# Kernel optimization log

Hardware: AMD Instinct MI355X
Metric: run time of the kernel (lower is better)

Reference implementation:

```python
import jax, jax.numpy as jnp
import numpy as np

N = 250_000        # nodes
E = 8_000_000      # directed edges
F_IN = 16          # dataset.num_features
H = 8              # latent_dim
G = 512            # number of graphs in the batch


def setup_inputs() -> dict:
    key = jax.random.key(0)
    k = jax.random.split(key, 9)
    x = jax.random.normal(k[0], (N, F_IN), dtype=jnp.float32)
    edge_index = jax.random.randint(k[1], (2, E), 0, N, dtype=jnp.int64)
    batch = jnp.sort(jax.random.randint(k[2], (N,), 0, G, dtype=jnp.int64))
    W1 = jax.random.normal(k[3], (F_IN, H), dtype=jnp.float32) * 0.25
    b1 = jax.random.normal(k[4], (H,), dtype=jnp.float32) * 0.1
    W2 = jax.random.normal(k[5], (H, H), dtype=jnp.float32) * 0.35
    b2 = jax.random.normal(k[6], (H,), dtype=jnp.float32) * 0.1
    Wl = jax.random.normal(k[7], (H, 1), dtype=jnp.float32) * 0.35
    bl = jax.random.normal(k[8], (1,), dtype=jnp.float32) * 0.1
    return {"x": x, "edge_index": edge_index, "batch": batch,
            "W1": W1, "b1": b1, "W2": W2, "b2": b2, "Wl": Wl, "bl": bl}


def _gcn_conv(x, src, dst, deg_inv_sqrt, W, b, num_nodes):
    # PyG GCNConv (default): h = x @ W ; msg = norm * h[src] ; scatter-add to dst ; + bias
    h = x @ W                                    # [N, H]
    norm = deg_inv_sqrt[src] * deg_inv_sqrt[dst]  # [E+N]
    msgs = h[src] * norm[:, None]                 # [E+N, H]
    out = jax.ops.segment_sum(msgs, dst, num_segments=num_nodes)
    return out + b


def reference(x, edge_index, batch, W1, b1, W2, b2, Wl, bl):
    num_nodes = x.shape[0]
    loops = jnp.arange(num_nodes, dtype=edge_index.dtype)
    src = jnp.concatenate([edge_index[0], loops])  # self-loops appended
    dst = jnp.concatenate([edge_index[1], loops])
    # symmetric normalization: deg over destination (incl. self-loops)
    deg = jax.ops.segment_sum(jnp.ones_like(dst, dtype=x.dtype), dst,
                              num_segments=num_nodes)
    dis = jnp.where(deg > 0, jax.lax.rsqrt(jnp.maximum(deg, 1.0)), 0.0)
    h = jax.nn.relu(_gcn_conv(x, src, dst, dis, W1, b1, num_nodes))
    h = jax.nn.relu(_gcn_conv(h, src, dst, dis, W2, b2, num_nodes))
    pooled = jax.ops.segment_sum(h, batch, num_segments=G)  # global_add_pool -> [G, H]
    return jax.nn.sigmoid(pooled @ Wl + bl)                 # [G, 1]
```

## Files before the change

kernel.cpp:

```cpp
#include <hip/hip_runtime.h>
#include <math.h>

#define BLK 256
#define CH 8192
#define NBMAX 1024


__global__ void k_init0(int* __restrict__ ghist, float* __restrict__ zacc,
                        int* __restrict__ rowptr, int nb, int ng, int n, int E,
                        int primary) {
  int i = blockIdx.x * BLK + threadIdx.x;
  if (i < nb) ghist[i] = 0;
  if (i < ng) zacc[i] = 0.f;
  if (primary && i == 0) rowptr[n] = E;
}

__global__ void k_hist(const int* __restrict__ dst, int* __restrict__ ghist,
                       int E, int nb, int chunk) {
  __shared__ int h[NBMAX];
  for (int i = threadIdx.x; i < NBMAX; i += BLK) h[i] = 0;
  __syncthreads();
  long long s0 = (long long)blockIdx.x * chunk;
  int c = (int)min((long long)chunk, (long long)E - s0);
  for (int i = threadIdx.x; i < c; i += BLK)
    atomicAdd(&h[dst[s0 + i] >> 8], 1);
  __syncthreads();
  for (int b = threadIdx.x; b < nb; b += BLK)
    if (h[b]) atomicAdd(&ghist[b], h[b]);
}

__global__ void k_scan(const int* __restrict__ ghist, int* __restrict__ base,
                       int* __restrict__ cursor, int nb, int E) {
  __shared__ int temp[BLK];
  int t = threadIdx.x;
  int v[4]; int sm = 0;
  #pragma unroll
  for (int k = 0; k < 4; ++k) {
    int idx = t * 4 + k;
    v[k] = (idx < nb) ? ghist[idx] : 0;
    sm += v[k];
  }
  temp[t] = sm; __syncthreads();
  int inc = sm;
  for (int off = 1; off < BLK; off <<= 1) {
    int u = (t >= off) ? temp[t - off] : 0; __syncthreads();
    inc += u; temp[t] = inc; __syncthreads();
  }
  int run = inc - sm;
  #pragma unroll
  for (int k = 0; k < 4; ++k) {
    int idx = t * 4 + k;
    if (idx < nb) { base[idx] = run; cursor[idx] = run; }
    run += v[k];
  }
  if (t == BLK - 1) base[nb] = E;
}

__global__ void k_bin(const int* __restrict__ src, const int* __restrict__ dst,
                      int* __restrict__ cursor, int* __restrict__ binned,
                      int E, int nb) {
  __shared__ int cnt[NBMAX], cur[NBMAX], gofs[NBMAX], baseA[NBMAX + 1], temp[BLK];
  __shared__ int stage[CH];
  int t = threadIdx.x;
  for (int i = t; i < NBMAX; i += BLK) { cnt[i] = 0; cur[i] = 0; }
  __syncthreads();
  long long s0 = (long long)blockIdx.x * CH;
  int c = (int)min((long long)CH, (long long)E - s0);
  for (int i = t; i < c; i += BLK) atomicAdd(&cnt[dst[s0 + i] >> 8], 1);
  __syncthreads();
  int v[4], sm = 0;
  #pragma unroll
  for (int k = 0; k < 4; ++k) { v[k] = cnt[t * 4 + k]; sm += v[k]; }
  temp[t] = sm; __syncthreads();
  int inc = sm;
  for (int off = 1; off < BLK; off <<= 1) {
    int u = (t >= off) ? temp[t - off] : 0; __syncthreads();
    inc += u; temp[t] = inc; __syncthreads();
  }
  int run = inc - sm;
  #pragma unroll
  for (int k = 0; k < 4; ++k) { baseA[t * 4 + k] = run; run += v[k]; }
  if (t == BLK - 1) baseA[NBMAX] = c;
  __syncthreads();
  for (int b = t; b < nb; b += BLK)
    if (cnt[b]) gofs[b] = atomicAdd(&cursor[b], cnt[b]);
  __syncthreads();
  for (int i = t; i < c; i += BLK) {
    int d = dst[s0 + i];
    int b = d >> 8;
    int r = atomicAdd(&cur[b], 1);
    stage[baseA[b] + r] = (src[s0 + i] << 8) | (d & 255);
  }
  __syncthreads();
  for (int i = t; i < c; i += BLK) {
    int lo = 0, hi = nb;
    while (hi - lo > 1) { int m = (lo + hi) >> 1; if (baseA[m] <= i) lo = m; else hi = m; }
    binned[(size_t)gofs[lo] + (i - baseA[lo])] = stage[i];
  }
}

__global__ void k_sortdis(const int* __restrict__ base, const int* __restrict__ binned,
                          int* __restrict__ csr, int* __restrict__ rowptr,
                          float* __restrict__ dis, int n) {
  __shared__ int cnt[256], loff[256], cur[256], temp[BLK];
  int b = blockIdx.x, t = threadIdx.x;
  cnt[t] = 0; cur[t] = 0;
  __syncthreads();
  int s = base[b], e = base[b + 1];
  for (int i = s + t; i < e; i += BLK) atomicAdd(&cnt[binned[i] & 255], 1);
  __syncthreads();
  int v = cnt[t];
  temp[t] = v; __syncthreads();
  int inc = v;
  for (int off = 1; off < BLK; off <<= 1) {
    int u = (t >= off) ? temp[t - off] : 0; __syncthreads();
    inc += u; temp[t] = inc; __syncthreads();
  }
  loff[t] = inc - v;
  int node = b * 256 + t;
  if (node < n) {
    rowptr[node] = s + inc - v;
    dis[node] = rsqrtf((float)(v + 1));
  }
  __syncthreads();
  for (int i = s + t; i < e; i += BLK) {
    int rec = binned[i];
    int L = rec & 255;
    int p = atomicAdd(&cur[L], 1);
    csr[s + loff[L] + p] = rec >> 8;
  }
}

__global__ void k_gather(const int* __restrict__ rowptr, const int* __restrict__ csr,
                         const float* __restrict__ y, float* __restrict__ acc, int n) {
  int t = blockIdx.x * BLK + threadIdx.x;
  int node = t >> 3;
  int h = t & 7;
  if (node >= n) return;
  int start = rowptr[node];
  int end = rowptr[node + 1];
  float s = 0.f;
  int si = (start < end) ? csr[start] : 0;
  for (int k = start; k < end; ++k) {
    int nsi = (k + 1 < end) ? csr[k + 1] : 0;
    s += y[(size_t)si * 8 + h];
    si = nsi;
  }
  acc[(size_t)node * 8 + h] = s;
}


__global__ void k_degdis(const int* __restrict__ base, const int* __restrict__ binned,
                         float* __restrict__ dis, int n) {
  __shared__ int deg[256];
  int b = blockIdx.x, t = threadIdx.x;
  deg[t] = 1;
  __syncthreads();
  int s = base[b], e = base[b + 1];
  for (int i = s + t; i < e; i += BLK) atomicAdd(&deg[binned[i] & 255], 1);
  __syncthreads();
  int node = b * 256 + t;
  if (node < n) dis[node] = rsqrtf((float)deg[t]);
}

__global__ void k_acc(const int* __restrict__ base, const int* __restrict__ binned,
                      const float* __restrict__ y, float* __restrict__ acc, int n) {
  __shared__ float fa[2048];
  int b = blockIdx.x, t = threadIdx.x;
  for (int i = t; i < 2048; i += BLK) fa[i] = 0.f;
  __syncthreads();
  int s = base[b], e = base[b + 1];
  int j = t & 7;
  for (int i = s + (t >> 3); i < e; i += 32) {
    int rec = binned[i];
    atomicAdd(&fa[(rec & 255) * 8 + j], y[(size_t)(rec >> 8) * 8 + j]);
  }
  __syncthreads();
  int node0 = b * 256;
  int lim = (n - node0 < 256 ? n - node0 : 256) * 8;
  for (int i = t; i < lim; i += BLK) acc[(size_t)node0 * 8 + i] = fa[i];
}


__global__ void k_y1n(const float* __restrict__ x, const float* __restrict__ W1,
                      const float* __restrict__ dis, float* __restrict__ y, int n) {
  __shared__ float sW[128];
  if (threadIdx.x < 128) sW[threadIdx.x] = W1[threadIdx.x];
  __syncthreads();
  int i = blockIdx.x * BLK + threadIdx.x;
  if (i >= n) return;
  const float4* xp = (const float4*)(x + (size_t)i * 16);
  float4 a = xp[0], bb = xp[1], cc = xp[2], d4 = xp[3];
  float xv[16] = {a.x,a.y,a.z,a.w, bb.x,bb.y,bb.z,bb.w,
                  cc.x,cc.y,cc.z,cc.w, d4.x,d4.y,d4.z,d4.w};
  float ds = dis[i];
  float o[8];
  #pragma unroll
  for (int jj = 0; jj < 8; ++jj) {
    float s = 0.f;
    #pragma unroll
    for (int k = 0; k < 16; ++k) s = fmaf(xv[k], sW[k*8 + jj], s);
    o[jj] = ds * s;
  }
  float4* yp = (float4*)(y + (size_t)i * 8);
  yp[0] = make_float4(o[0], o[1], o[2], o[3]);
  yp[1] = make_float4(o[4], o[5], o[6], o[7]);
}

__global__ void k_mid(const float* __restrict__ dis, float* __restrict__ y,
                      float* __restrict__ acc, const float* __restrict__ W2,
                      const float* __restrict__ b1, int n, int zero_acc) {
  __shared__ float sW[64];
  __shared__ float sb[8];
  if (threadIdx.x < 64) sW[threadIdx.x] = W2[threadIdx.x];
  if (threadIdx.x < 8)  sb[threadIdx.x] = b1[threadIdx.x];
  __syncthreads();
  int i = blockIdx.x * BLK + threadIdx.x;
  if (i >= n) return;
  float d = dis[i];
  float4* yp = (float4*)(y + (size_t)i * 8);
  float4* ap = (float4*)(acc + (size_t)i * 8);
  float4 y0 = yp[0], y1v = yp[1], a0 = ap[0], a1 = ap[1];
  float yy[8] = {y0.x,y0.y,y0.z,y0.w, y1v.x,y1v.y,y1v.z,y1v.w};
  float aa[8] = {a0.x,a0.y,a0.z,a0.w, a1.x,a1.y,a1.z,a1.w};
  float hv[8];
  #pragma unroll
  for (int jj = 0; jj < 8; ++jj) hv[jj] = fmaxf(fmaf(d, yy[jj] + aa[jj], sb[jj]), 0.f);
  float o[8];
  #pragma unroll
  for (int jj = 0; jj < 8; ++jj) {
    float s = 0.f;
    #pragma unroll
    for (int k = 0; k < 8; ++k) s = fmaf(hv[k], sW[k*8 + jj], s);
    o[jj] = d * s;
  }
  yp[0] = make_float4(o[0], o[1], o[2], o[3]);
  yp[1] = make_float4(o[4], o[5], o[6], o[7]);
  if (zero_acc) {
    ap[0] = make_float4(0.f, 0.f, 0.f, 0.f);
    ap[1] = make_float4(0.f, 0.f, 0.f, 0.f);
  }
}

__global__ void k_final(const float* __restrict__ dis, const float* __restrict__ y,
                        const float* __restrict__ acc, const float* __restrict__ b2,
                        const float* __restrict__ Wl, const int* __restrict__ batch,
                        float* __restrict__ zacc, int n) {
  __shared__ float sb[8], sw[8];
  if (threadIdx.x < 8) { sb[threadIdx.x] = b2[threadIdx.x]; sw[threadIdx.x] = Wl[threadIdx.x]; }
  __syncthreads();
  int i = blockIdx.x * BLK + threadIdx.x;
  float s = 0.f;
  int g = -1;
  if (i < n) {
    float d = dis[i];
    const float4* yp = (const float4*)(y + (size_t)i * 8);
    const float4* ap = (const float4*)(acc + (size_t)i * 8);
    float4 y0 = yp[0], y1v = yp[1], a0 = ap[0], a1 = ap[1];
    float yy[8] = {y0.x,y0.y,y0.z,y0.w, y1v.x,y1v.y,y1v.z,y1v.w};
    float aa[8] = {a0.x,a0.y,a0.z,a0.w, a1.x,a1.y,a1.z,a1.w};
    #pragma unroll
    for (int jj = 0; jj < 8; ++jj) {
      float h = fmaxf(fmaf(d, yy[jj] + aa[jj], sb[jj]), 0.f);
      s = fmaf(h, sw[jj], s);
    }
    g = batch[i];
  }
  int g0 = __shfl(g, 0);
  bool uni = __all(g == g0);
  if (uni) {
    #pragma unroll
    for (int off = 32; off > 0; off >>= 1) s += __shfl_down(s, off);
    if ((threadIdx.x & 63) == 0 && g0 >= 0) unsafeAtomicAdd(&zacc[g0], s);
  } else if (i < n) {
    unsafeAtomicAdd(&zacc[g], s);
  }
}

__global__ void k_out(const float* __restrict__ zacc, const float* __restrict__ bl,
                      float* __restrict__ out, int ng) {
  int i = blockIdx.x * BLK + threadIdx.x;
  if (i < ng) {
    float z = zacc[i] + bl[0];
    float r;
    if (z >= 0.f) { r = 1.f / (1.f + expf(-z)); }
    else          { float e = expf(z); r = e / (1.f + e); }
    out[i] = r;
  }
}


__global__ void k_init(int* __restrict__ deg, float* __restrict__ acc,
                       float* __restrict__ zacc, int n, int accn, int ng) {
  int jj = blockIdx.x * BLK + threadIdx.x;
  if (jj < accn) acc[jj] = 0.f;
  if (jj < n) deg[jj] = 1;
  if (jj < ng) zacc[jj] = 0.f;
}

__global__ void k_deg(const int* __restrict__ dst, int* __restrict__ deg, int E) {
  int i = blockIdx.x * BLK + threadIdx.x;
  if (i < E) atomicAdd(&deg[dst[i]], 1);
}

__global__ void k_y1(const float* __restrict__ x, const float* __restrict__ W1,
                     int* __restrict__ degdis, float* __restrict__ y, int n) {
  __shared__ float sW[128];
  if (threadIdx.x < 128) sW[threadIdx.x] = W1[threadIdx.x];
  __syncthreads();
  int i = blockIdx.x * BLK + threadIdx.x;
  if (i >= n) return;
  const float4* xp = (const float4*)(x + (size_t)i * 16);
  float4 a = xp[0], bb = xp[1], cc = xp[2], d4 = xp[3];
  float xv[16] = {a.x,a.y,a.z,a.w, bb.x,bb.y,bb.z,bb.w,
                  cc.x,cc.y,cc.z,cc.w, d4.x,d4.y,d4.z,d4.w};
  float ds = rsqrtf((float)degdis[i]);
  float o[8];
  #pragma unroll
  for (int jj = 0; jj < 8; ++jj) {
    float s = 0.f;
    #pragma unroll
    for (int k = 0; k < 16; ++k) s = fmaf(xv[k], sW[k*8 + jj], s);
    o[jj] = ds * s;
  }
  ((float*)degdis)[i] = ds;
  float4* yp = (float4*)(y + (size_t)i * 8);
  yp[0] = make_float4(o[0], o[1], o[2], o[3]);
  yp[1] = make_float4(o[4], o[5], o[6], o[7]);
}

__global__ void k_scatter(const int* __restrict__ src, const int* __restrict__ dst,
                          const float* __restrict__ y, float* __restrict__ acc,
                          long long total) {
  long long t = (long long)blockIdx.x * BLK + threadIdx.x;
  if (t >= total) return;
  int e = (int)(t >> 3);
  int h = (int)(t & 7);
  int s = src[e], d = dst[e];
  unsafeAtomicAdd(&acc[(size_t)d * 8 + h], y[(size_t)s * 8 + h]);
}


static inline size_t alignup(size_t v) { return (v + 255) & ~(size_t)255; }

extern "C" void kernel_launch(void* const* d_in, const int* in_sizes, int n_in,
                              void* d_out, int out_size, void* d_ws, size_t ws_size,
                              hipStream_t stream) {
  const float* x   = (const float*)d_in[0];
  const int*   ei  = (const int*)  d_in[1];
  const int*   bat = (const int*)  d_in[2];
  const float* W1  = (const float*)d_in[3];
  const float* b1  = (const float*)d_in[4];
  const float* W2  = (const float*)d_in[5];
  const float* b2  = (const float*)d_in[6];
  const float* Wl  = (const float*)d_in[7];
  const float* bl  = (const float*)d_in[8];
  float* out = (float*)d_out;

  int n  = in_sizes[0] / 16;
  int E  = in_sizes[1] / 2;
  int ng = out_size;

  const int* src = ei;
  const int* dst = ei + E;

  int nb = (n + 255) >> 8;

  char* wsb = (char*)d_ws;
  size_t offY  = alignup((size_t)n * 4);
  size_t offA  = offY + alignup((size_t)n * 8 * 4);
  size_t offZ  = offA + alignup((size_t)n * 8 * 4);
  size_t offH  = offZ + alignup((size_t)ng * 4);
  size_t offB  = offH + alignup((size_t)NBMAX * 4);
  size_t offCu = offB + alignup((size_t)(NBMAX + 1) * 4);
  size_t offBn = offCu + alignup((size_t)NBMAX * 4);
  size_t offRp = offBn + alignup((size_t)E * 4);
  size_t offCs = offRp + alignup(((size_t)n + 1) * 4);
  size_t need1 = offCs + alignup((size_t)E * 4);
  size_t need2 = offRp;

  float* dis    = (float*)wsb;
  int*   deg    = (int*)wsb;
  float* y      = (float*)(wsb + offY);
  float* acc    = (float*)(wsb + offA);
  float* zacc   = (float*)(wsb + offZ);
  int*   ghist  = (int*)(wsb + offH);
  int*   base   = (int*)(wsb + offB);
  int*   cursor = (int*)(wsb + offCu);
  int*   binned = (int*)(wsb + offBn);
  int*   rowptr = (int*)(wsb + offRp);
  int*   csr    = (int*)(wsb + offCs);

  int gN = (n + BLK - 1) / BLK;
  int gG = (ng + BLK - 1) / BLK;
  int gT = (n * 8 + BLK - 1) / BLK;

  bool ok_bin = (nb <= NBMAX) && (n < (1 << 23));
  bool tier1 = ok_bin && (ws_size >= need1);
  bool tier2 = ok_bin && (ws_size >= need2);

  if (tier1 || tier2) {
    int histChunk = 15625;
    int gHist = (int)(((long long)E + histChunk - 1) / histChunk);
    int gBin  = (int)(((long long)E + CH - 1) / CH);
    int gI0   = (NBMAX > ng ? NBMAX : ng) / BLK + 1;
    k_init0 <<<gI0, BLK, 0, stream>>>(ghist, zacc, rowptr, NBMAX, ng, n, E, tier1 ? 1 : 0);
    k_hist  <<<gHist, BLK, 0, stream>>>(dst, ghist, E, nb, histChunk);
    k_scan  <<<1, BLK, 0, stream>>>(ghist, base, cursor, nb, E);
    k_bin   <<<gBin, BLK, 0, stream>>>(src, dst, cursor, binned, E, nb);
    if (tier1) {
      k_sortdis<<<nb, BLK, 0, stream>>>(base, binned, csr, rowptr, dis, n);
      k_y1n   <<<gN, BLK, 0, stream>>>(x, W1, dis, y, n);
      k_gather<<<gT, BLK, 0, stream>>>(rowptr, csr, y, acc, n);
      k_mid   <<<gN, BLK, 0, stream>>>(dis, y, acc, W2, b1, n, 0);
      k_gather<<<gT, BLK, 0, stream>>>(rowptr, csr, y, acc, n);
    } else {
      k_degdis<<<nb, BLK, 0, stream>>>(base, binned, dis, n);
      k_y1n   <<<gN, BLK, 0, stream>>>(x, W1, dis, y, n);
      k_acc   <<<nb, BLK, 0, stream>>>(base, binned, y, acc, n);
      k_mid   <<<gN, BLK, 0, stream>>>(dis, y, acc, W2, b1, n, 0);
      k_acc   <<<nb, BLK, 0, stream>>>(base, binned, y, acc, n);
    }
    k_final <<<gN, BLK, 0, stream>>>(dis, y, acc, b2, Wl, bat, zacc, n);
  } else {
    int accn = n * 8;
    long long tot = (long long)E * 8;
    int gInit = (accn + BLK - 1) / BLK;
    int gE    = (E + BLK - 1) / BLK;
    int gS    = (int)((tot + BLK - 1) / BLK);
    k_init   <<<gInit, BLK, 0, stream>>>(deg, acc, zacc, n, accn, ng);
    k_deg    <<<gE, BLK, 0, stream>>>(dst, deg, E);
    k_y1     <<<gN, BLK, 0, stream>>>(x, W1, deg, y, n);
    k_scatter<<<gS, BLK, 0, stream>>>(src, dst, y, acc, tot);
    k_mid    <<<gN, BLK, 0, stream>>>(dis, y, acc, W2, b1, n, 1);
    k_scatter<<<gS, BLK, 0, stream>>>(src, dst, y, acc, tot);
    k_final  <<<gN, BLK, 0, stream>>>(dis, y, acc, b2, Wl, bat, zacc, n);
  }
  k_out<<<gG, BLK, 0, stream>>>(zacc, bl, out, ng);
}
```

Baseline: 537.5 us.

## Use warp-per-node gather and drop LDS staging in edge binning

The gather kernel now assigns one 64-lane wavefront per node, with 8 edge slots times 8 features, and reduces across the edge slots using shuffles. Before, it used 8 threads per node and walked each neighbor list serially, which gave a long dependent latency chain for nodes with about 32 edges. The binning kernel drops its prefix-scan, LDS staging and binary-search scatter, and writes each record straight to its global slot. That saves LDS traffic and syncs, but the global writes are less coalesced.

```diff
diff --git a/kernel.cpp b/kernel.cpp
--- a/kernel.cpp
+++ b/kernel.cpp
@@ -59,28 +59,13 @@
 __global__ void k_bin(const int* __restrict__ src, const int* __restrict__ dst,
                       int* __restrict__ cursor, int* __restrict__ binned,
                       int E, int nb) {
-  __shared__ int cnt[NBMAX], cur[NBMAX], gofs[NBMAX], baseA[NBMAX + 1], temp[BLK];
-  __shared__ int stage[CH];
+  __shared__ int cnt[NBMAX], cur[NBMAX], gofs[NBMAX];
   int t = threadIdx.x;
   for (int i = t; i < NBMAX; i += BLK) { cnt[i] = 0; cur[i] = 0; }
   __syncthreads();
   long long s0 = (long long)blockIdx.x * CH;
   int c = (int)min((long long)CH, (long long)E - s0);
   for (int i = t; i < c; i += BLK) atomicAdd(&cnt[dst[s0 + i] >> 8], 1);
-  __syncthreads();
-  int v[4], sm = 0;
-  #pragma unroll
-  for (int k = 0; k < 4; ++k) { v[k] = cnt[t * 4 + k]; sm += v[k]; }
-  temp[t] = sm; __syncthreads();
-  int inc = sm;
-  for (int off = 1; off < BLK; off <<= 1) {
-    int u = (t >= off) ? temp[t - off] : 0; __syncthreads();
-    inc += u; temp[t] = inc; __syncthreads();
-  }
-  int run = inc - sm;
-  #pragma unroll
-  for (int k = 0; k < 4; ++k) { baseA[t * 4 + k] = run; run += v[k]; }
-  if (t == BLK - 1) baseA[NBMAX] = c;
   __syncthreads();
   for (int b = t; b < nb; b += BLK)
     if (cnt[b]) gofs[b] = atomicAdd(&cursor[b], cnt[b]);
@@ -89,13 +74,7 @@
     int d = dst[s0 + i];
     int b = d >> 8;
     int r = atomicAdd(&cur[b], 1);
-    stage[baseA[b] + r] = (src[s0 + i] << 8) | (d & 255);
-  }
-  __syncthreads();
-  for (int i = t; i < c; i += BLK) {
-    int lo = 0, hi = nb;
-    while (hi - lo > 1) { int m = (lo + hi) >> 1; if (baseA[m] <= i) lo = m; else hi = m; }
-    binned[(size_t)gofs[lo] + (i - baseA[lo])] = stage[i];
+    binned[(size_t)gofs[b] + r] = (src[s0 + i] << 8) | (d & 255);
   }
 }
 
@@ -133,20 +112,25 @@
 
 __global__ void k_gather(const int* __restrict__ rowptr, const int* __restrict__ csr,
                          const float* __restrict__ y, float* __restrict__ acc, int n) {
-  int t = blockIdx.x * BLK + threadIdx.x;
-  int node = t >> 3;
-  int h = t & 7;
-  if (node >= n) return;
-  int start = rowptr[node];
-  int end = rowptr[node + 1];
+  int wid = (int)(((long long)blockIdx.x * BLK + threadIdx.x) >> 6);
+  if (wid >= n) return;
+  int lane = threadIdx.x & 63;
+  int e = lane & 7, h = lane >> 3;
+  int start = rowptr[wid], end = rowptr[wid + 1];
   float s = 0.f;
-  int si = (start < end) ? csr[start] : 0;
-  for (int k = start; k < end; ++k) {
-    int nsi = (k + 1 < end) ? csr[k + 1] : 0;
-    s += y[(size_t)si * 8 + h];
-    si = nsi;
-  }
-  acc[(size_t)node * 8 + h] = s;
+  int k0 = start;
+  int k = k0 + e;
+  int sidx = (k < end) ? csr[k] : -1;
+  while (k0 < end) {
+    int nk = k0 + 8 + e;
+    int nsidx = (nk < end) ? csr[nk] : -1;
+    if (sidx >= 0) s += y[(size_t)sidx * 8 + h];
+    sidx = nsidx; k0 += 8;
+  }
+  s += __shfl_xor(s, 1);
+  s += __shfl_xor(s, 2);
+  s += __shfl_xor(s, 4);
+  if (e == 0) acc[(size_t)wid * 8 + h] = s;
 }
 
 
@@ -393,7 +377,7 @@
 
   int gN = (n + BLK - 1) / BLK;
   int gG = (ng + BLK - 1) / BLK;
-  int gT = (n * 8 + BLK - 1) / BLK;
+  int gW = (int)(((long long)n * 64 + BLK - 1) / BLK);
 
   bool ok_bin = (nb <= NBMAX) && (n < (1 << 23));
   bool tier1 = ok_bin && (ws_size >= need1);
@@ -411,9 +395,9 @@
     if (tier1) {
       k_sortdis<<<nb, BLK, 0, stream>>>(base, binned, csr, rowptr, dis, n);
       k_y1n   <<<gN, BLK, 0, stream>>>(x, W1, dis, y, n);
-      k_gather<<<gT, BLK, 0, stream>>>(rowptr, csr, y, acc, n);
+      k_gather<<<gW, BLK, 0, stream>>>(rowptr, csr, y, acc, n);
       k_mid   <<<gN, BLK, 0, stream>>>(dis, y, acc, W2, b1, n, 0);
-      k_gather<<<gT, BLK, 0, stream>>>(rowptr, csr, y, acc, n);
+      k_gather<<<gW, BLK, 0, stream>>>(rowptr, csr, y, acc, n);
     } else {
       k_degdis<<<nb, BLK, 0, stream>>>(base, binned, dis, n);
       k_y1n   <<<gN, BLK, 0, stream>>>(x, W1, dis, y, n);
```

New measurement: 549.3 us. 1.02x slower.
